# Kernel tuning notes

Hardware: AMD Instinct MI355X
Metric: run time of the kernel (lower is better)

Reference implementation:

```python
import jax, jax.numpy as jnp
import numpy as np


def setup_inputs() -> dict:
    key = jax.random.key(0)
    k1, k2, k3, k4, k5 = jax.random.split(key, 5)
    B, T, H = 32, 4096, 256
    D = 2 * H  # encoder feature dim
    hidden = jax.random.normal(k1, (B, D), dtype=jnp.float32)
    encoder_outputs = jax.random.normal(k2, (B, T, D), dtype=jnp.float32)
    # torch nn.Linear(4H, H): weight [H, 4H], bias [H]
    W_attn = jax.random.normal(k3, (H, 4 * H), dtype=jnp.float32) * (1.0 / np.sqrt(4 * H))
    b_attn = jax.random.normal(k4, (H,), dtype=jnp.float32) * 0.01
    v = jax.random.uniform(k5, (H,), dtype=jnp.float32)  # torch.rand init
    return {"hidden": hidden, "encoder_outputs": encoder_outputs,
            "W_attn": W_attn, "b_attn": b_attn, "v": v}


def reference(hidden, encoder_outputs, W_attn, b_attn, v):
    D = hidden.shape[-1]  # 2*H
    # Split Linear(4H->H) weight into the hidden part and encoder part so we
    # never materialize the [B,T,4H] concat: cat(h,e) @ W.T == h @ Wh.T + e @ We.T
    W_h = W_attn[:, :D]   # [H, 2H]
    W_e = W_attn[:, D:]   # [H, 2H]
    h_proj = hidden @ W_h.T                     # [B, H]
    e_proj = jnp.einsum('btd,hd->bth', encoder_outputs, W_e)  # [B, T, H]
    energy = jnp.tanh(h_proj[:, None, :] + e_proj + b_attn)   # [B, T, H]
    scores = energy @ v                          # [B, T]
    attn_weights = jax.nn.softmax(scores, axis=1)  # softmax over timesteps
    context = jnp.einsum('bt,btd->bd', attn_weights, encoder_outputs)  # [B, 2H]
    return context, attn_weights
```

## Files before the change

kernel.cpp:

```cpp
#include <hip/hip_runtime.h>
#include <hip/hip_bf16.h>
#include <math.h>

#define B_  32
#define T_  4096
#define H_  256
#define D_  512

#define WS_PRE    0
#define WS_WEHI   32768
#define WS_P      294912
#define WS_ML     819200
#define WS_PCTX   835584

using short8  = __attribute__((ext_vector_type(8))) short;
using float4v = __attribute__((ext_vector_type(4))) float;

__device__ __forceinline__ unsigned cvt2_bf16(float lo, float hi) {
    union { __hip_bfloat162 h; unsigned u; } cv;
    cv.h = __float22bfloat162_rn(make_float2(lo, hi));
    return cv.u;
}
__device__ __forceinline__ uint2 cvt4_bf16(const float* a) {
    return make_uint2(cvt2_bf16(a[0], a[1]), cvt2_bf16(a[2], a[3]));
}

__device__ __forceinline__ float bf16_to_f32(unsigned short u) {
    return __uint_as_float(((unsigned)u) << 16);
}

__device__ __forceinline__ float fast_tanh(float x) {
    float e = __expf(2.0f * x);
    return 1.0f - 2.0f * __builtin_amdgcn_rcpf(e + 1.0f);
}

__global__ __launch_bounds__(256)
void prep_kernel(const float* __restrict__ hidden,
                 const float* __restrict__ W_attn,
                 const float* __restrict__ b_attn,
                 unsigned char* __restrict__ ws) {
    int blk = blockIdx.x;
    int tid = threadIdx.x;
    if (blk < 32) {
        int b = blk, h = tid;
        const float4* hv = (const float4*)(hidden + b * D_);
        const float4* wv = (const float4*)(W_attn + (size_t)h * 1024);
        float s = 0.f;
        #pragma unroll 4
        for (int d4 = 0; d4 < D_ / 4; ++d4) {
            float4 a = hv[d4], w = wv[d4];
            s += a.x * w.x + a.y * w.y + a.z * w.z + a.w * w.w;
        }
        ((float*)(ws + WS_PRE))[b * H_ + h] = s + b_attn[h];
    } else {
        int q = (blk - 32) * 256 + tid;
        unsigned short* whi = (unsigned short*)(ws + WS_WEHI);
        #pragma unroll
        for (int i = 0; i < 4; ++i) {
            int idx4 = q + i * 8192;
            int n = idx4 >> 7, k = (idx4 & 127) << 2;
            int t = k >> 5, kin = k & 31;
            int quad = kin >> 3, e = kin & 7;
            int slot = quad ^ ((n >> 1) & 3);
            float4 w = *(const float4*)(W_attn + (size_t)n * 1024 + 512 + k);
            unsigned lo = cvt2_bf16(w.x, w.y);
            unsigned hi = cvt2_bf16(w.z, w.w);
            unsigned short* dst = whi + t * 8192 + n * 32 + slot * 8 + e;
            *(uint2*)dst = make_uint2(lo, hi);
        }
    }
}

#define BM 64
#define BN 256
#define BK 32
#define LDT 520
#define KIT 16

__global__ __launch_bounds__(512, 4)
void gemm_scores_kernel(const float* __restrict__ enc,
                        unsigned char* __restrict__ ws,
                        const float* __restrict__ v) {
    __shared__ unsigned short sE[BM * LDT];
    __shared__ float sScoreP[4][BM];
    __shared__ float sP[BM];

    const float*          pre = (const float*)(ws + WS_PRE);
    const unsigned short* weh = (const unsigned short*)(ws + WS_WEHI);

    int tid = threadIdx.x;
    int m0  = blockIdx.x * BM;
    int b   = m0 >> 12;

    int rowA = tid >> 3, c8 = (tid & 7) * 4;
    const float* gA = enc + (size_t)(m0 + rowA) * D_ + c8;

    int wave = tid >> 6, lane = tid & 63;
    int wm = wave & 1, wn = wave >> 1;
    int quad = lane >> 4, l16 = lane & 15;

    int slotB = quad ^ ((l16 >> 1) & 3);
    const unsigned short* bBase = weh + (wn * 64 + l16) * 32 + slotB * 8;

    float4v acc[2][4] = {};

    float aX[4], aY[4];
    short8 bhA[4], bhB[4];

    {
        float4 x0 = *(const float4*)gA;
        #pragma unroll
        for (int j = 0; j < 4; ++j)
            bhA[j] = *(const short8*)(bBase + j * 512);
        float4 y0 = *(const float4*)(gA + BK);
        #pragma unroll
        for (int j = 0; j < 4; ++j)
            bhB[j] = *(const short8*)(bBase + 8192 + j * 512);

        float tmp[4];
        *(float4*)tmp = x0;
        *(uint2*)&sE[rowA * LDT + c8] = cvt4_bf16(tmp);
        *(float4*)aY = y0;
    }
    __builtin_amdgcn_s_waitcnt(0xc07f);
    __builtin_amdgcn_s_barrier();

#define K_STEP(kk, Acons, Aload, Bcur, Bnxt)                                  \
    {                                                                         \
        if ((kk) + 1 < KIT) {                                                 \
            const unsigned short* pb = bBase + ((kk) + 1) * 8192;             \
            Bnxt[0] = *(const short8*)(pb);                                   \
            Bnxt[1] = *(const short8*)(pb + 512);                             \
            Bnxt[2] = *(const short8*)(pb + 1024);                            \
            Bnxt[3] = *(const short8*)(pb + 1536);                            \
        }                                                                     \
        if ((kk) + 2 < KIT) {                                                 \
            *(float4*)(Aload) = *(const float4*)(gA + ((kk) + 2) * BK);       \
        }                                                                     \
        short8 ah[2];                                                         \
        _Pragma("unroll")                                                     \
        for (int i = 0; i < 2; ++i) {                                         \
            int r = wm * 32 + i * 16 + l16;                                   \
            ah[i] = *(const short8*)&sE[r * LDT + (kk) * BK + quad * 8];      \
        }                                                                     \
        _Pragma("unroll")                                                     \
        for (int i = 0; i < 2; ++i)                                           \
            _Pragma("unroll")                                                 \
            for (int j = 0; j < 4; ++j)                                       \
                acc[i][j] = __builtin_amdgcn_mfma_f32_16x16x32_bf16(          \
                    ah[i], Bcur[j], acc[i][j], 0, 0, 0);                      \
        if ((kk) + 1 < KIT) {                                                 \
            *(uint2*)&sE[rowA * LDT + ((kk) + 1) * BK + c8] =                 \
                cvt4_bf16(Acons);                                             \
            __builtin_amdgcn_s_waitcnt(0xc07f);                               \
            __builtin_amdgcn_s_barrier();                                     \
        }                                                                     \
    }

    for (int kt = 0; kt < 8; ++kt) {
        K_STEP(2 * kt,     aY, aX, bhA, bhB)
        K_STEP(2 * kt + 1, aX, aY, bhB, bhA)
    }
#undef K_STEP

    float rowsum[2][4] = {};
    #pragma unroll
    for (int j = 0; j < 4; ++j) {
        int n = wn * 64 + j * 16 + l16;
        float pv = pre[b * H_ + n];
        float vv = v[n];
        #pragma unroll
        for (int i = 0; i < 2; ++i)
            #pragma unroll
            for (int r = 0; r < 4; ++r)
                rowsum[i][r] += fast_tanh(acc[i][j][r] + pv) * vv;
    }
    #pragma unroll
    for (int i = 0; i < 2; ++i)
        #pragma unroll
        for (int r = 0; r < 4; ++r) {
            float s = rowsum[i][r];
            s += __shfl_xor(s, 1);
            s += __shfl_xor(s, 2);
            s += __shfl_xor(s, 4);
            s += __shfl_xor(s, 8);
            rowsum[i][r] = s;
        }
    if (l16 == 0) {
        #pragma unroll
        for (int i = 0; i < 2; ++i)
            #pragma unroll
            for (int r = 0; r < 4; ++r) {
                int row = wm * 32 + i * 16 + quad * 4 + r;
                sScoreP[wn][row] = rowsum[i][r];
            }
    }
    __syncthreads();

    if (tid < 64) {
        float sval = sScoreP[0][tid] + sScoreP[1][tid]
                   + sScoreP[2][tid] + sScoreP[3][tid];
        float m = sval;
        #pragma unroll
        for (int off = 32; off; off >>= 1) m = fmaxf(m, __shfl_xor(m, off));
        float p = expf(sval - m);
        sP[tid] = p;
        ((float*)(ws + WS_P))[m0 + tid] = p;
        float l = p;
        #pragma unroll
        for (int off = 32; off; off >>= 1) l += __shfl_xor(l, off);
        if (tid == 0)
            ((float2*)(ws + WS_ML))[blockIdx.x] = make_float2(m, l);
    }
    __syncthreads();

    int colg = tid & 127, rgrp = tid >> 7;
    float4 c4 = {0.f, 0.f, 0.f, 0.f};
    #pragma unroll 4
    for (int s = 0; s < 16; ++s) {
        int r = rgrp + 4 * s;
        float w = sP[r];
        uint2 raw = *(const uint2*)&sE[r * LDT + colg * 4];
        c4.x += w * bf16_to_f32((unsigned short)(raw.x & 0xffffu));
        c4.y += w * bf16_to_f32((unsigned short)(raw.x >> 16));
        c4.z += w * bf16_to_f32((unsigned short)(raw.y & 0xffffu));
        c4.w += w * bf16_to_f32((unsigned short)(raw.y >> 16));
    }
    __syncthreads();
    float4* red4 = (float4*)sE;
    red4[tid] = c4;
    __syncthreads();
    if (rgrp == 0) {
        float4 a0 = red4[colg], a1 = red4[colg + 128];
        float4 a2 = red4[colg + 256], a3 = red4[colg + 384];
        float4 o;
        o.x = a0.x + a1.x + a2.x + a3.x;
        o.y = a0.y + a1.y + a2.y + a3.y;
        o.z = a0.z + a1.z + a2.z + a3.z;
        o.w = a0.w + a1.w + a2.w + a3.w;
        ((float4*)(ws + WS_PCTX))[blockIdx.x * 128 + colg] = o;
    }
}

__global__ __launch_bounds__(512)
void finalize_kernel(const unsigned char* __restrict__ ws,
                     float* __restrict__ out_ctx,
                     float* __restrict__ out_w) {
    __shared__ float sm[64], sl[64], sscale[64];
    int b = blockIdx.x, tid = threadIdx.x;
    const float2* ml  = ((const float2*)(ws + WS_ML)) + b * 64;
    if (tid < 64) {
        float2 v = ml[tid];
        sm[tid] = v.x; sl[tid] = v.y;
    }
    __syncthreads();
    float m = -1e30f;
    #pragma unroll
    for (int i = 0; i < 64; ++i) m = fmaxf(m, sm[i]);
    float l = 0.f;
    #pragma unroll
    for (int i = 0; i < 64; ++i) l += sl[i] * expf(sm[i] - m);
    float inv = 1.0f / l;
    if (tid < 64) sscale[tid] = expf(sm[tid] - m) * inv;
    __syncthreads();

    {
        const float4* pb = (const float4*)((const float*)(ws + WS_P) + (size_t)b * T_);
        float4* wb = (float4*)(out_w + (size_t)b * T_);
        int t0 = tid * 2;
        float sc = sscale[tid >> 3];
        float4 x = pb[t0], y = pb[t0 + 1];
        x.x *= sc; x.y *= sc; x.z *= sc; x.w *= sc;
        y.x *= sc; y.y *= sc; y.z *= sc; y.w *= sc;
        wb[t0] = x; wb[t0 + 1] = y;
    }
    {
        const float* pc = (const float*)(ws + WS_PCTX) + (size_t)b * 64 * D_;
        float c = 0.f;
        #pragma unroll
        for (int i = 0; i < 64; ++i) c += pc[i * D_ + tid] * sscale[i];
        out_ctx[b * D_ + tid] = c;
    }
}

extern "C" void kernel_launch(void* const* d_in, const int* in_sizes, int n_in,
                              void* d_out, int out_size, void* d_ws, size_t ws_size,
                              hipStream_t stream) {
    const float* hidden = (const float*)d_in[0];
    const float* enc    = (const float*)d_in[1];
    const float* W_attn = (const float*)d_in[2];
    const float* b_attn = (const float*)d_in[3];
    const float* v      = (const float*)d_in[4];
    float* out = (float*)d_out;
    unsigned char* ws = (unsigned char*)d_ws;

    prep_kernel<<<64, 256, 0, stream>>>(hidden, W_attn, b_attn, ws);
    gemm_scores_kernel<<<T_ * B_ / BM, 512, 0, stream>>>(enc, ws, v);
    finalize_kernel<<<B_, 512, 0, stream>>>(ws, out, out + B_ * D_);
}
```

Measured before the change: 397.4 us.

## Halve barriers in GEMM main loop by staging two K-tiles per sync

Restructures the K loop of the scores GEMM so that each iteration converts and stores two 32-wide K slices of the encoder tile into shared memory, then issues a single barrier, instead of one barrier per slice. The next A prefetch and both B fragment loads are rescheduled around this. The aim is to cut barrier and waitcnt stalls. The cost is a shorter prefetch distance for the B fragments, since bhB is now loaded just before its use, and that latency is less hidden.

Result: no change. 397.5 us (+0.0%).

```diff
diff --git a/kernel.cpp b/kernel.cpp
--- a/kernel.cpp
+++ b/kernel.cpp
@@ -75,7 +75,6 @@
 #define BN 256
 #define BK 32
 #define LDT 520
-#define KIT 16
 
 __global__ __launch_bounds__(512, 4)
 void gemm_scores_kernel(const float* __restrict__ enc,
@@ -107,61 +106,67 @@
     float aX[4], aY[4];
     short8 bhA[4], bhB[4];
 
-    {
-        float4 x0 = *(const float4*)gA;
-        #pragma unroll
-        for (int j = 0; j < 4; ++j)
-            bhA[j] = *(const short8*)(bBase + j * 512);
-        float4 y0 = *(const float4*)(gA + BK);
-        #pragma unroll
-        for (int j = 0; j < 4; ++j)
-            bhB[j] = *(const short8*)(bBase + 8192 + j * 512);
-
-        float tmp[4];
-        *(float4*)tmp = x0;
-        *(uint2*)&sE[rowA * LDT + c8] = cvt4_bf16(tmp);
-        *(float4*)aY = y0;
-    }
+    *(float4*)aX = *(const float4*)gA;
+    *(float4*)aY = *(const float4*)(gA + BK);
+    #pragma unroll
+    for (int j = 0; j < 4; ++j)
+        bhA[j] = *(const short8*)(bBase + j * 512);
+    *(uint2*)&sE[rowA * LDT + c8]      = cvt4_bf16(aX);
+    *(uint2*)&sE[rowA * LDT + BK + c8] = cvt4_bf16(aY);
     __builtin_amdgcn_s_waitcnt(0xc07f);
     __builtin_amdgcn_s_barrier();
-
-#define K_STEP(kk, Acons, Aload, Bcur, Bnxt)                                  \
-    {                                                                         \
-        if ((kk) + 1 < KIT) {                                                 \
-            const unsigned short* pb = bBase + ((kk) + 1) * 8192;             \
-            Bnxt[0] = *(const short8*)(pb);                                   \
-            Bnxt[1] = *(const short8*)(pb + 512);                             \
-            Bnxt[2] = *(const short8*)(pb + 1024);                            \
-            Bnxt[3] = *(const short8*)(pb + 1536);                            \
-        }                                                                     \
-        if ((kk) + 2 < KIT) {                                                 \
-            *(float4*)(Aload) = *(const float4*)(gA + ((kk) + 2) * BK);       \
-        }                                                                     \
-        short8 ah[2];                                                         \
-        _Pragma("unroll")                                                     \
-        for (int i = 0; i < 2; ++i) {                                         \
-            int r = wm * 32 + i * 16 + l16;                                   \
-            ah[i] = *(const short8*)&sE[r * LDT + (kk) * BK + quad * 8];      \
-        }                                                                     \
-        _Pragma("unroll")                                                     \
-        for (int i = 0; i < 2; ++i)                                           \
-            _Pragma("unroll")                                                 \
-            for (int j = 0; j < 4; ++j)                                       \
-                acc[i][j] = __builtin_amdgcn_mfma_f32_16x16x32_bf16(          \
-                    ah[i], Bcur[j], acc[i][j], 0, 0, 0);                      \
-        if ((kk) + 1 < KIT) {                                                 \
-            *(uint2*)&sE[rowA * LDT + ((kk) + 1) * BK + c8] =                 \
-                cvt4_bf16(Acons);                                             \
-            __builtin_amdgcn_s_waitcnt(0xc07f);                               \
-            __builtin_amdgcn_s_barrier();                                     \
-        }                                                                     \
-    }
-
-    for (int kt = 0; kt < 8; ++kt) {
-        K_STEP(2 * kt,     aY, aX, bhA, bhB)
-        K_STEP(2 * kt + 1, aX, aY, bhB, bhA)
-    }
-#undef K_STEP
+    *(float4*)aX = *(const float4*)(gA + 2 * BK);
+    *(float4*)aY = *(const float4*)(gA + 3 * BK);
+
+    #pragma unroll
+    for (int t = 0; t < 8; ++t) {
+        {
+            const unsigned short* pb = bBase + (2 * t + 1) * 8192;
+            #pragma unroll
+            for (int j = 0; j < 4; ++j)
+                bhB[j] = *(const short8*)(pb + j * 512);
+        }
+        short8 ah[2];
+        #pragma unroll
+        for (int i = 0; i < 2; ++i) {
+            int r = wm * 32 + i * 16 + l16;
+            ah[i] = *(const short8*)&sE[r * LDT + (2 * t) * BK + quad * 8];
+        }
+        #pragma unroll
+        for (int i = 0; i < 2; ++i)
+            #pragma unroll
+            for (int j = 0; j < 4; ++j)
+                acc[i][j] = __builtin_amdgcn_mfma_f32_16x16x32_bf16(
+                    ah[i], bhA[j], acc[i][j], 0, 0, 0);
+        #pragma unroll
+        for (int i = 0; i < 2; ++i) {
+            int r = wm * 32 + i * 16 + l16;
+            ah[i] = *(const short8*)&sE[r * LDT + (2 * t + 1) * BK + quad * 8];
+        }
+        #pragma unroll
+        for (int i = 0; i < 2; ++i)
+            #pragma unroll
+            for (int j = 0; j < 4; ++j)
+                acc[i][j] = __builtin_amdgcn_mfma_f32_16x16x32_bf16(
+                    ah[i], bhB[j], acc[i][j], 0, 0, 0);
+
+        if (t < 7) {
+            *(uint2*)&sE[rowA * LDT + (2 * t + 2) * BK + c8] = cvt4_bf16(aX);
+            *(uint2*)&sE[rowA * LDT + (2 * t + 3) * BK + c8] = cvt4_bf16(aY);
+            if (t < 6) {
+                *(float4*)aX = *(const float4*)(gA + (2 * t + 4) * BK);
+                *(float4*)aY = *(const float4*)(gA + (2 * t + 5) * BK);
+            }
+            {
+                const unsigned short* pb = bBase + (2 * t + 2) * 8192;
+                #pragma unroll
+                for (int j = 0; j < 4; ++j)
+                    bhA[j] = *(const short8*)(pb + j * 512);
+            }
+            __builtin_amdgcn_s_waitcnt(0xc07f);
+            __builtin_amdgcn_s_barrier();
+        }
+    }
 
     float rowsum[2][4] = {};
     #pragma unroll
```
